# Optimization experiments

Measured on AMD Instinct MI355X. Metric: run time of the kernel, lower is better.

The kernel has to match this reference:

```python
import jax, jax.numpy as jnp
import numpy as np

N_EMBD = 768
N_HEAD = 12
B, T = 2, 2048


def setup_inputs() -> dict:
    key = jax.random.key(0)
    ks = jax.random.split(key, 8)
    C = N_EMBD
    s = 0.02
    return {
        "x": jax.random.normal(ks[0], (B, T, C), jnp.float32),
        "ln1_g": jnp.ones((C,), jnp.float32),
        "ln1_b": jnp.zeros((C,), jnp.float32),
        "w_attn": jax.random.normal(ks[1], (C, 3 * C), jnp.float32) * s,
        "b_attn": jnp.zeros((3 * C,), jnp.float32),
        "w_attn_proj": jax.random.normal(ks[2], (C, C), jnp.float32) * s,
        "b_attn_proj": jnp.zeros((C,), jnp.float32),
        "ln2_g": jnp.ones((C,), jnp.float32),
        "ln2_b": jnp.zeros((C,), jnp.float32),
        "w_fc": jax.random.normal(ks[3], (C, 4 * C), jnp.float32) * s,
        "b_fc": jnp.zeros((4 * C,), jnp.float32),
        "w_mlp_proj": jax.random.normal(ks[4], (4 * C, C), jnp.float32) * s,
        "b_mlp_proj": jnp.zeros((C,), jnp.float32),
    }


def _layernorm(x, g, b, eps=1e-5):
    mu = jnp.mean(x, axis=-1, keepdims=True)
    var = jnp.mean(jnp.square(x - mu), axis=-1, keepdims=True)
    return (x - mu) * jax.lax.rsqrt(var + eps) * g + b


def _new_gelu(x):
    c = np.sqrt(2.0 / np.pi).astype(np.float32)
    return 0.5 * x * (1.0 + jnp.tanh(c * (x + 0.044715 * x * x * x)))


def _block(x, ln1_g, ln1_b, w_attn, b_attn, w_attn_proj, b_attn_proj,
           ln2_g, ln2_b, w_fc, b_fc, w_mlp_proj, b_mlp_proj):
    Bx, Tx, C = x.shape
    hd = C // N_HEAD
    h = _layernorm(x, ln1_g, ln1_b)
    qkv = h @ w_attn + b_attn  # [B,T,3C]
    q, k, v = jnp.split(qkv, 3, axis=-1)
    # [B,H,T,hd]
    q = q.reshape(Bx, Tx, N_HEAD, hd).transpose(0, 2, 1, 3)
    k = k.reshape(Bx, Tx, N_HEAD, hd).transpose(0, 2, 1, 3)
    v = v.reshape(Bx, Tx, N_HEAD, hd).transpose(0, 2, 1, 3)
    att = jnp.einsum('bhqd,bhkd->bhqk', q, k) * (1.0 / np.sqrt(hd))
    causal = jnp.tril(jnp.ones((Tx, Tx), bool))
    att = jnp.where(causal[None, None], att, -jnp.inf)
    att = jax.nn.softmax(att, axis=-1)
    y = jnp.einsum('bhqk,bhkd->bhqd', att, v)
    y = y.transpose(0, 2, 1, 3).reshape(Bx, Tx, C)
    x = x + y @ w_attn_proj + b_attn_proj
    h2 = _layernorm(x, ln2_g, ln2_b)
    x = x + _new_gelu(h2 @ w_fc + b_fc) @ w_mlp_proj + b_mlp_proj
    return x


def reference(x, ln1_g, ln1_b, w_attn, b_attn, w_attn_proj, b_attn_proj,
              ln2_g, ln2_b, w_fc, b_fc, w_mlp_proj, b_mlp_proj):
    return _block(x, ln1_g, ln1_b, w_attn, b_attn, w_attn_proj, b_attn_proj,
                  ln2_g, ln2_b, w_fc, b_fc, w_mlp_proj, b_mlp_proj)
```

## Files before the change

### kernel.cpp

```cpp
#include <hip/hip_runtime.h>
#include <hip/hip_bf16.h>
#include <math.h>

#define N_EMBD 768
#define N_HEAD 12
#define BATCH  2
#define SEQ    2048
#define ROWS   (BATCH*SEQ)
#define C3     (3*N_EMBD)

typedef __bf16 bf16;
typedef __attribute__((ext_vector_type(8))) __bf16 bf16x8;
typedef __attribute__((ext_vector_type(4))) float f32x4;

__device__ __forceinline__ void async16(const bf16* g, bf16* l) {
    __builtin_amdgcn_global_load_lds(
        (const __attribute__((address_space(1))) uint32_t*)g,
        (__attribute__((address_space(3))) uint32_t*)l, 16, 0, 0);
}

__global__ __launch_bounds__(256) void k_transpose_all(
    const float* __restrict__ w0, bf16* __restrict__ o0,
    const float* __restrict__ w1, bf16* __restrict__ o1,
    const float* __restrict__ w2, bf16* __restrict__ o2,
    const float* __restrict__ w3, bf16* __restrict__ o3)
{
    __shared__ bf16 tile[32][33];
    int bid = blockIdx.x;
    const float* in; bf16* out; int K, N, local;
    if      (bid < 1728) { in = w0; out = o0; K = 768;  N = 2304; local = bid; }
    else if (bid < 2304) { in = w1; out = o1; K = 768;  N = 768;  local = bid - 1728; }
    else if (bid < 4608) { in = w2; out = o2; K = 768;  N = 3072; local = bid - 2304; }
    else                 { in = w3; out = o3; K = 3072; N = 768;  local = bid - 4608; }
    int nt = N / 32;
    int n0 = (local % nt) * 32, k0 = (local / nt) * 32;
    int tc = threadIdx.x & 31, tr = threadIdx.x >> 5;
    #pragma unroll
    for (int i = 0; i < 4; i++) {
        int r = tr + i * 8;
        tile[r][tc] = (bf16)in[(size_t)(k0 + r) * N + n0 + tc];
    }
    __syncthreads();
    #pragma unroll
    for (int i = 0; i < 4; i++) {
        int r = tr + i * 8;
        out[(size_t)(n0 + r) * K + k0 + tc] = tile[tc][r];
    }
}

__global__ __launch_bounds__(256) void k_layernorm(
    const float* __restrict__ x, const float* __restrict__ g,
    const float* __restrict__ b, bf16* __restrict__ out)
{
    int wave = threadIdx.x >> 6, lane = threadIdx.x & 63;
    int row = blockIdx.x * 4 + wave;
    const float* xr = x + (size_t)row * N_EMBD;
    float v[12];
    float s = 0.f, sq = 0.f;
    #pragma unroll
    for (int i = 0; i < 12; i++) {
        v[i] = xr[lane + 64 * i];
        s += v[i]; sq += v[i] * v[i];
    }
    #pragma unroll
    for (int off = 32; off > 0; off >>= 1) {
        s  += __shfl_xor(s, off);
        sq += __shfl_xor(sq, off);
    }
    float mu  = s * (1.f / N_EMBD);
    float var = sq * (1.f / N_EMBD) - mu * mu;
    float rs  = rsqrtf(var + 1e-5f);
    bf16* orow = out + (size_t)row * N_EMBD;
    #pragma unroll
    for (int i = 0; i < 12; i++) {
        int c = lane + 64 * i;
        orow[c] = (bf16)((v[i] - mu) * rs * g[c] + b[c]);
    }
}

template<int BN, int ACT, bool RES, bool OUT_BF16, bool VOUT>
__global__ __launch_bounds__(256) void k_gemm(
    const bf16* __restrict__ A, const bf16* __restrict__ Bt,
    const float* __restrict__ bias, const float* __restrict__ res,
    void* __restrict__ outp, bf16* __restrict__ vout, int M, int N, int K)
{
    constexpr int WC  = BN / 64;
    constexpr int WR  = 4 / WC;
    constexpr int RPW = 128 / WR;
    constexpr int MI  = RPW / 16;
    __shared__ __align__(16) bf16 As[128 * 64];
    __shared__ __align__(16) bf16 Bs[BN * 64];
    int n0 = blockIdx.x * BN, m0 = blockIdx.y * 128;
    int t = threadIdx.x;
    int lane = t & 63, wave = t >> 6;
    int wr = wave / WC, wc = wave % WC;
    int quad = lane >> 4, l16 = lane & 15;

    f32x4 acc[MI][4];
    #pragma unroll
    for (int i = 0; i < MI; i++)
        #pragma unroll
        for (int j = 0; j < 4; j++) acc[i][j] = (f32x4){0.f, 0.f, 0.f, 0.f};

    int sr = t >> 3;
    int sc = t & 7;
    int gsw = (sc ^ (sr & 7)) * 8;

    for (int k0 = 0; k0 < K; k0 += 64) {
        __syncthreads();
        #pragma unroll
        for (int p = 0; p < 4; p++) {
            int r = sr + p * 32;
            async16(&A[(size_t)(m0 + r) * K + k0 + gsw], &As[r * 64 + sc * 8]);
        }
        #pragma unroll
        for (int p = 0; p < BN / 32; p++) {
            int r = sr + p * 32;
            async16(&Bt[(size_t)(n0 + r) * K + k0 + gsw], &Bs[r * 64 + sc * 8]);
        }
        __syncthreads();
        #pragma unroll
        for (int kh = 0; kh < 2; kh++) {
            bf16x8 af[MI], bfv[4];
            #pragma unroll
            for (int i = 0; i < MI; i++)
                af[i]  = *(bf16x8*)&As[(wr * RPW + i * 16 + l16) * 64 + (((quad + 4 * kh) ^ (l16 & 7)) * 8)];
            #pragma unroll
            for (int j = 0; j < 4; j++)
                bfv[j] = *(bf16x8*)&Bs[(wc * 64 + j * 16 + l16) * 64 + (((quad + 4 * kh) ^ (l16 & 7)) * 8)];
            #pragma unroll
            for (int i = 0; i < MI; i++)
                #pragma unroll
                for (int j = 0; j < 4; j++)
                    acc[i][j] = __builtin_amdgcn_mfma_f32_16x16x32_bf16(af[i], bfv[j], acc[i][j], 0, 0, 0);
        }
    }

    if (VOUT && n0 >= 1536) {
        #pragma unroll
        for (int i = 0; i < MI; i++) {
            #pragma unroll
            for (int j = 0; j < 4; j++) {
                int col = n0 + wc * 64 + j * 16 + l16;
                int hv = (col - 1536) >> 6, dv = (col - 1536) & 63;
                float bv = bias[col];
                int row0 = m0 + wr * RPW + i * 16 + quad * 4;
                int bb = row0 >> 11, ts = row0 & 2047;
                union { ushort4 u4; bf16 e[4]; } pk;
                #pragma unroll
                for (int r = 0; r < 4; r++) pk.e[r] = (bf16)(acc[i][j][r] + bv);
                *(ushort4*)&vout[((size_t)(bb * N_HEAD + hv) * 64 + dv) * SEQ + ts] = pk.u4;
            }
        }
        return;
    }

    float* outf = (float*)outp;
    bf16*  outb = (bf16*)outp;
    #pragma unroll
    for (int i = 0; i < MI; i++) {
        #pragma unroll
        for (int j = 0; j < 4; j++) {
            int col = n0 + wc * 64 + j * 16 + l16;
            float bv = bias[col];
            #pragma unroll
            for (int r = 0; r < 4; r++) {
                int row = m0 + wr * RPW + i * 16 + quad * 4 + r;
                float v = acc[i][j][r] + bv;
                if (ACT == 1) {
                    float z = 0.7978845608f * (v + 0.044715f * v * v * v);
                    v = v / (1.f + __expf(-2.f * z));
                }
                if (RES) v += res[(size_t)row * N + col];
                if (OUT_BF16) outb[(size_t)row * N + col] = (bf16)v;
                else          outf[(size_t)row * N + col] = v;
            }
        }
    }
}

#define PS_S 72
__global__ __launch_bounds__(256) void k_flash(
    const bf16* __restrict__ qkv, const bf16* __restrict__ vt, bf16* __restrict__ y)
{
    __shared__ __align__(16) bf16 Ks[2][64 * 64];
    __shared__ __align__(16) bf16 VTl[2][64 * 64];
    __shared__ __align__(16) bf16 Ps[4][16 * PS_S];
    int bid = blockIdx.x;
    int u = bid >> 1, sb = bid & 1;
    int v = u & 31, w = u >> 5;
    int bh = 2 * w + sb;
    int qt = sb ? 31 - v : v;
    int b = bh / N_HEAD, h = bh % N_HEAD;
    int t = threadIdx.x, lane = t & 63, wave = t >> 6;
    int quad = lane >> 4, l16 = lane & 15;
    int qbase = qt * 64 + wave * 16;

    bf16x8 qa[2];
    {
        const bf16* qrow = qkv + (size_t)(b * SEQ + qbase + l16) * C3 + h * 64;
        #pragma unroll
        for (int kh = 0; kh < 2; kh++) {
            union { uint4 u4; bf16 e[8]; bf16x8 vv; } uq;
            uq.u4 = *(const uint4*)&qrow[quad * 8 + kh * 32];
            #pragma unroll
            for (int j = 0; j < 8; j++) uq.e[j] = (bf16)((float)uq.e[j] * 0.125f);
            qa[kh] = uq.vv;
        }
    }
    float l_part[4] = {0.f, 0.f, 0.f, 0.f};
    f32x4 o[4];
    #pragma unroll
    for (int j = 0; j < 4; j++) o[j] = (f32x4){0.f, 0.f, 0.f, 0.f};

    int sr = t >> 3;
    int sc = t & 7;
    int gsw = (sc ^ (sr & 7)) * 8;

    const bf16* kg = qkv + (size_t)b * SEQ * C3 + N_EMBD + h * 64;
    const bf16* vg = vt + (size_t)bh * 64 * SEQ;

    auto stage = [&](int tile, int bufi) {
        int k0 = tile * 64;
        #pragma unroll
        for (int p = 0; p < 2; p++) {
            int rr = sr + 32 * p;
            async16(&kg[(size_t)(k0 + rr) * C3 + gsw],  &Ks[bufi][rr * 64 + sc * 8]);
            async16(&vg[(size_t)rr * SEQ + k0 + gsw], &VTl[bufi][rr * 64 + sc * 8]);
        }
    };

    int ntiles = qt + 1;
    stage(0, 0);

    for (int tt = 0; tt < ntiles; tt++) {
        int bufi = tt & 1;
        int k0 = tt * 64;
        __syncthreads();
        if (tt + 1 < ntiles) stage(tt + 1, bufi ^ 1);

        f32x4 s[4];
        #pragma unroll
        for (int nt = 0; nt < 4; nt++) {
            bf16x8 b0 = *(bf16x8*)&Ks[bufi][(nt * 16 + l16) * 64 + (((quad    ) ^ (l16 & 7)) * 8)];
            bf16x8 b1 = *(bf16x8*)&Ks[bufi][(nt * 16 + l16) * 64 + (((quad + 4) ^ (l16 & 7)) * 8)];
            f32x4 z = (f32x4){0.f, 0.f, 0.f, 0.f};
            z = __builtin_amdgcn_mfma_f32_16x16x32_bf16(qa[0], b0, z, 0, 0, 0);
            z = __builtin_amdgcn_mfma_f32_16x16x32_bf16(qa[1], b1, z, 0, 0, 0);
            s[nt] = z;
        }
        bool diag = (tt == qt);
        float p[4][4];
        #pragma unroll
        for (int nt = 0; nt < 4; nt++) {
            int key = k0 + nt * 16 + l16;
            #pragma unroll
            for (int r = 0; r < 4; r++) {
                float pv = __expf(s[nt][r]);
                if (diag && key > qbase + quad * 4 + r) pv = 0.f;
                p[nt][r] = pv;
                l_part[r] += pv;
            }
        }
        #pragma unroll
        for (int nt = 0; nt < 4; nt++)
            #pragma unroll
            for (int r = 0; r < 4; r++)
                Ps[wave][(quad * 4 + r) * PS_S + nt * 16 + l16] = (bf16)p[nt][r];
        bf16x8 pa[2];
        #pragma unroll
        for (int kt = 0; kt < 2; kt++)
            pa[kt] = *(bf16x8*)&Ps[wave][l16 * PS_S + kt * 32 + quad * 8];
        #pragma unroll
        for (int jt = 0; jt < 4; jt++) {
            int d = jt * 16 + l16;
            #pragma unroll
            for (int kt = 0; kt < 2; kt++) {
                bf16x8 vb = *(bf16x8*)&VTl[bufi][d * 64 + (((quad + 4 * kt) ^ (l16 & 7)) * 8)];
                o[jt] = __builtin_amdgcn_mfma_f32_16x16x32_bf16(pa[kt], vb, o[jt], 0, 0, 0);
            }
        }
    }
    #pragma unroll
    for (int r = 0; r < 4; r++) {
        #pragma unroll
        for (int off = 8; off > 0; off >>= 1) l_part[r] += __shfl_xor(l_part[r], off);
    }
    #pragma unroll
    for (int jt = 0; jt < 4; jt++)
        #pragma unroll
        for (int r = 0; r < 4; r++) {
            int q = qbase + quad * 4 + r;
            y[(size_t)(b * SEQ + q) * N_EMBD + h * 64 + jt * 16 + l16] =
                (bf16)(o[jt][r] / l_part[r]);
        }
}

extern "C" void kernel_launch(void* const* d_in, const int* in_sizes, int n_in,
                              void* d_out, int out_size, void* d_ws, size_t ws_size,
                              hipStream_t stream) {
    const float* x           = (const float*)d_in[0];
    const float* ln1_g       = (const float*)d_in[1];
    const float* ln1_b       = (const float*)d_in[2];
    const float* w_attn      = (const float*)d_in[3];
    const float* b_attn      = (const float*)d_in[4];
    const float* w_attn_proj = (const float*)d_in[5];
    const float* b_attn_proj = (const float*)d_in[6];
    const float* ln2_g       = (const float*)d_in[7];
    const float* ln2_b       = (const float*)d_in[8];
    const float* w_fc        = (const float*)d_in[9];
    const float* b_fc        = (const float*)d_in[10];
    const float* w_mlp_proj  = (const float*)d_in[11];
    const float* b_mlp_proj  = (const float*)d_in[12];

    char* ws = (char*)d_ws;
    size_t off = 0;
    auto alloc = [&](size_t n) -> void* {
        off = (off + 255) & ~(size_t)255;
        void* p = ws + off;
        off += n;
        return p;
    };
    bf16* wqkvT  = (bf16*)alloc((size_t)C3 * N_EMBD * 2);
    bf16* wprojT = (bf16*)alloc((size_t)N_EMBD * N_EMBD * 2);
    bf16* wfcT   = (bf16*)alloc((size_t)4 * N_EMBD * N_EMBD * 2);
    bf16* wmlpT  = (bf16*)alloc((size_t)N_EMBD * 4 * N_EMBD * 2);
    bf16* hbuf   = (bf16*)alloc((size_t)ROWS * N_EMBD * 2);
    float* x2    = (float*)alloc((size_t)ROWS * N_EMBD * 4);
    bf16* yb     = (bf16*)alloc((size_t)ROWS * N_EMBD * 2);
    bf16* vtb    = (bf16*)alloc((size_t)BATCH * N_HEAD * 64 * SEQ * 2);
    bf16* big    = (bf16*)alloc((size_t)ROWS * 4 * N_EMBD * 2);
    bf16* qkvb   = big;
    bf16* actb   = big;

    k_transpose_all<<<6912, 256, 0, stream>>>(w_attn, wqkvT, w_attn_proj, wprojT,
                                              w_fc, wfcT, w_mlp_proj, wmlpT);

    k_layernorm<<<ROWS / 4, 256, 0, stream>>>(x, ln1_g, ln1_b, hbuf);
    k_gemm<128, 0, false, true,  true ><<<dim3(C3 / 128,  ROWS / 128), 256, 0, stream>>>(
        hbuf, wqkvT,  b_attn,      nullptr, qkvb, vtb,     ROWS, C3,     N_EMBD);
    k_flash<<<768, 256, 0, stream>>>(qkvb, vtb, yb);
    k_gemm<64,  0, true,  false, false><<<dim3(N_EMBD / 64, ROWS / 128), 256, 0, stream>>>(
        yb,   wprojT, b_attn_proj, x,       x2,   nullptr, ROWS, N_EMBD, N_EMBD);
    k_layernorm<<<ROWS / 4, 256, 0, stream>>>(x2, ln2_g, ln2_b, hbuf);
    k_gemm<128, 1, false, true,  false><<<dim3(3072 / 128, ROWS / 128), 256, 0, stream>>>(
        hbuf, wfcT,   b_fc,        nullptr, actb, nullptr, ROWS, 3072,   N_EMBD);
    k_gemm<64,  0, true,  false, false><<<dim3(N_EMBD / 64, ROWS / 128), 256, 0, stream>>>(
        actb, wmlpT,  b_mlp_proj,  x2, (float*)d_out, nullptr, ROWS, N_EMBD, 3072);
}
```

Measured before the change: 304.0 us.

## Move V transpose to separate kernel and remap flash block schedule

Removes the fused V-transpose epilogue from the QKV GEMM and adds a standalone LDS-tiled transpose kernel that reads V from the qkv buffer. It also changes how flash-attention block IDs map to (batch-head, query tile), interleaving 8 heads per group with a staggered query-tile order to balance causal work across CUs. The cost is an extra launch and an extra read and write of V, traded for a GEMM epilogue without scattered stores and possibly better load balance in the attention kernel.

```diff
diff --git a/kernel.cpp b/kernel.cpp
--- a/kernel.cpp
+++ b/kernel.cpp
@@ -48,6 +48,28 @@
     }
 }
 
+__global__ __launch_bounds__(256) void k_vtrans(
+    const bf16* __restrict__ qkv, bf16* __restrict__ vt)
+{
+    __shared__ bf16 tile[32][33];
+    int tt = blockIdx.x;
+    int bh = blockIdx.y;
+    int dt = blockIdx.z;
+    int b = bh / N_HEAD, h = bh % N_HEAD;
+    int tc = threadIdx.x & 31, tr = threadIdx.x >> 5;
+    #pragma unroll
+    for (int i = 0; i < 4; i++) {
+        int r = tr + i * 8;
+        tile[r][tc] = qkv[(size_t)(b * SEQ + tt * 32 + r) * C3 + 2 * N_EMBD + h * 64 + dt * 32 + tc];
+    }
+    __syncthreads();
+    #pragma unroll
+    for (int i = 0; i < 4; i++) {
+        int r = tr + i * 8;
+        vt[(size_t)(bh * 64 + dt * 32 + r) * SEQ + tt * 32 + tc] = tile[tc][r];
+    }
+}
+
 __global__ __launch_bounds__(256) void k_layernorm(
     const float* __restrict__ x, const float* __restrict__ g,
     const float* __restrict__ b, bf16* __restrict__ out)
@@ -78,11 +100,11 @@
     }
 }
 
-template<int BN, int ACT, bool RES, bool OUT_BF16, bool VOUT>
+template<int BN, int ACT, bool RES, bool OUT_BF16>
 __global__ __launch_bounds__(256) void k_gemm(
     const bf16* __restrict__ A, const bf16* __restrict__ Bt,
     const float* __restrict__ bias, const float* __restrict__ res,
-    void* __restrict__ outp, bf16* __restrict__ vout, int M, int N, int K)
+    void* __restrict__ outp, int M, int N, int K)
 {
     constexpr int WC  = BN / 64;
     constexpr int WR  = 4 / WC;
@@ -136,25 +158,6 @@
         }
     }
 
-    if (VOUT && n0 >= 1536) {
-        #pragma unroll
-        for (int i = 0; i < MI; i++) {
-            #pragma unroll
-            for (int j = 0; j < 4; j++) {
-                int col = n0 + wc * 64 + j * 16 + l16;
-                int hv = (col - 1536) >> 6, dv = (col - 1536) & 63;
-                float bv = bias[col];
-                int row0 = m0 + wr * RPW + i * 16 + quad * 4;
-                int bb = row0 >> 11, ts = row0 & 2047;
-                union { ushort4 u4; bf16 e[4]; } pk;
-                #pragma unroll
-                for (int r = 0; r < 4; r++) pk.e[r] = (bf16)(acc[i][j][r] + bv);
-                *(ushort4*)&vout[((size_t)(bb * N_HEAD + hv) * 64 + dv) * SEQ + ts] = pk.u4;
-            }
-        }
-        return;
-    }
-
     float* outf = (float*)outp;
     bf16*  outb = (bf16*)outp;
     #pragma unroll
@@ -187,10 +190,15 @@
     __shared__ __align__(16) bf16 VTl[2][64 * 64];
     __shared__ __align__(16) bf16 Ps[4][16 * PS_S];
     int bid = blockIdx.x;
-    int u = bid >> 1, sb = bid & 1;
-    int v = u & 31, w = u >> 5;
-    int bh = 2 * w + sb;
-    int qt = sb ? 31 - v : v;
+    int hi = bid >> 8;
+    int lo = bid & 255;
+    int g  = lo >> 3;
+    int e  = lo & 7;
+    int bh = hi * 8 + e;
+    int qt;
+    if      (hi == 0) qt = g;
+    else if (hi == 1) qt = (g + 16) & 31;
+    else              qt = (g < 16) ? (30 - 2 * g) : (63 - 2 * g);
     int b = bh / N_HEAD, h = bh % N_HEAD;
     int t = threadIdx.x, lane = t & 63, wave = t >> 6;
     int quad = lane >> 4, l16 = lane & 15;
@@ -337,14 +345,15 @@
                                               w_fc, wfcT, w_mlp_proj, wmlpT);
 
     k_layernorm<<<ROWS / 4, 256, 0, stream>>>(x, ln1_g, ln1_b, hbuf);
-    k_gemm<128, 0, false, true,  true ><<<dim3(C3 / 128,  ROWS / 128), 256, 0, stream>>>(
-        hbuf, wqkvT,  b_attn,      nullptr, qkvb, vtb,     ROWS, C3,     N_EMBD);
+    k_gemm<128, 0, false, true ><<<dim3(C3 / 128,  ROWS / 128), 256, 0, stream>>>(
+        hbuf, wqkvT,  b_attn,      nullptr, qkvb, ROWS, C3,     N_EMBD);
+    k_vtrans<<<dim3(SEQ / 32, BATCH * N_HEAD, 2), 256, 0, stream>>>(qkvb, vtb);
     k_flash<<<768, 256, 0, stream>>>(qkvb, vtb, yb);
-    k_gemm<64,  0, true,  false, false><<<dim3(N_EMBD / 64, ROWS / 128), 256, 0, stream>>>(
-        yb,   wprojT, b_attn_proj, x,       x2,   nullptr, ROWS, N_EMBD, N_EMBD);
+    k_gemm<64,  0, true,  false><<<dim3(N_EMBD / 64, ROWS / 128), 256, 0, stream>>>(
+        yb,   wprojT, b_attn_proj, x,       x2,   ROWS, N_EMBD, N_EMBD);
     k_layernorm<<<ROWS / 4, 256, 0, stream>>>(x2, ln2_g, ln2_b, hbuf);
-    k_gemm<128, 1, false, true,  false><<<dim3(3072 / 128, ROWS / 128), 256, 0, stream>>>(
-        hbuf, wfcT,   b_fc,        nullptr, actb, nullptr, ROWS, 3072,   N_EMBD);
-    k_gemm<64,  0, true,  false, false><<<dim3(N_EMBD / 64, ROWS / 128), 256, 0, stream>>>(
-        actb, wmlpT,  b_mlp_proj,  x2, (float*)d_out, nullptr, ROWS, N_EMBD, 3072);
-}
+    k_gemm<128, 1, false, true ><<<dim3(3072 / 128, ROWS / 128), 256, 0, stream>>>(
+        hbuf, wfcT,   b_fc,        nullptr, actb, ROWS, 3072,   N_EMBD);
+    k_gemm<64,  0, true,  false><<<dim3(N_EMBD / 64, ROWS / 128), 256, 0, stream>>>(
+        actb, wmlpT,  b_mlp_proj,  x2, (float*)d_out, ROWS, N_EMBD, 3072);
+}
```

After: 288.7 us. 5.0% less time.
